# Optimization experiments

Measured on AMD Instinct MI355X. Metric: run time of the kernel, lower is better.

Reference implementation:

```python
import jax, jax.numpy as jnp
import numpy as np

N, G, E, R = 32768, 2048, 1146880, 3
NIN, GIN, F, OUT = 6, 4, 64, 1


def _w(k, fan_in, fan_out):
    return (jax.random.normal(k, (fan_in, fan_out), jnp.float32) / np.sqrt(fan_in)).astype(jnp.float32)


def setup_inputs() -> dict:
    key = jax.random.key(0)
    ks = jax.random.split(key, 20)
    x = jax.random.normal(ks[0], (N, NIN), jnp.float32)
    u = jax.random.normal(ks[1], (G, GIN), jnp.float32)
    batch = jnp.sort(jax.random.randint(ks[2], (N,), 0, G))
    hyperedge_index = jax.random.randint(ks[3], (R, E), 0, N)
    batch_hyper = jnp.sort(jax.random.randint(ks[4], (E,), 0, G))
    inp = {
        "x": x, "u": u, "batch": batch,
        "hyperedge_index": hyperedge_index, "batch_hyper": batch_hyper, "r": R,
        # mlp_x: (NIN+GIN)->F->F->F
        "W1": _w(ks[5], NIN + GIN, F), "b1": jnp.zeros((F,), jnp.float32),
        "W2": _w(ks[6], F, F), "b2": jnp.zeros((F,), jnp.float32),
        "W3": _w(ks[7], F, F), "b3": jnp.zeros((F,), jnp.float32),
        # weighting matrix [F,F]
        "weight": _w(ks[8], F, F),
        # x_hat: 2F->F->F->OUT
        "V1": _w(ks[9], 2 * F, F), "c1": jnp.zeros((F,), jnp.float32),
        "V2": _w(ks[10], F, F), "c2": jnp.zeros((F,), jnp.float32),
        "V3": _w(ks[11], F, OUT), "c3": jnp.zeros((OUT,), jnp.float32),
    }
    return inp


def _segment_softmax(x, idx, num_segments):
    # torch_geometric-style softmax grouped by idx along dim 0, per feature
    seg_max = jax.ops.segment_max(x, idx, num_segments=num_segments)
    ex = jnp.exp(x - seg_max[idx])
    denom = jax.ops.segment_sum(ex, idx, num_segments=num_segments)
    return ex / denom[idx]


def reference(x, u, batch, hyperedge_index, batch_hyper, r,
              W1, b1, W2, b2, W3, b3, weight, V1, c1, V2, c2, V3, c3):
    # mlp_x on [node_feats || global_feats_of_node's_graph]
    h = jnp.concatenate([x, u[batch]], axis=1)            # [N, NIN+GIN]
    h = jnp.maximum(h @ W1 + b1, 0.0)
    h = jnp.maximum(h @ W2 + b2, 0.0)
    h = h @ W3 + b3                                        # [N, F]

    # hyperedge finding: sum the r member-node embeddings of each hyperedge
    x_hyper = jnp.zeros((hyperedge_index.shape[1], h.shape[1]), h.dtype)
    for i in range(hyperedge_index.shape[0]):              # r is small & fixed
        x_hyper = x_hyper + jnp.take(h, hyperedge_index[i], axis=0)  # [E, F]

    # weighting: segment softmax over hyperedges of the same graph
    coef = _segment_softmax(x_hyper, batch_hyper, G)       # [E, F]
    x_hyper_hat = coef * jnp.maximum(x_hyper @ weight, 0.0)

    # x_hat head
    o = jnp.concatenate([x_hyper, x_hyper_hat], axis=1)    # [E, 2F]
    o = jnp.maximum(o @ V1 + c1, 0.0)
    o = jnp.maximum(o @ V2 + c2, 0.0)
    o = jax.nn.sigmoid(o @ V3 + c3)                        # [E, OUT]
    return (o, batch_hyper)
```

## Files before the change

### kernel.cpp

```cpp
#include <hip/hip_runtime.h>
#include <math.h>

typedef short bf16x8 __attribute__((ext_vector_type(8)));
typedef float f32x4  __attribute__((ext_vector_type(4)));
typedef unsigned short u16;
typedef unsigned int   u32;

#define MFMA16 __builtin_amdgcn_mfma_f32_16x16x32_bf16

__device__ __forceinline__ u16 f2b(float x) {
    union { float f; unsigned u; } v; v.f = x;
    unsigned r = v.u + 0x7fffu + ((v.u >> 16) & 1u);
    return (u16)(r >> 16);
}
__device__ __forceinline__ float b2f(u16 h) {
    union { unsigned u; float f; } v; v.u = ((unsigned)h) << 16;
    return v.f;
}
__device__ __forceinline__ float blo(u32 w) {
    union { u32 u; float f; } v; v.u = w << 16; return v.f;
}
__device__ __forceinline__ float bhi(u32 w) {
    union { u32 u; float f; } v; v.u = w & 0xffff0000u; return v.f;
}
__device__ __forceinline__ u32 add3pack(u32 x, u32 y, u32 z) {
    float lo = blo(x) + blo(y) + blo(z);
    float hi = bhi(x) + bhi(y) + bhi(z);
    return (u32)f2b(lo) | ((u32)f2b(hi) << 16);
}

__global__ __launch_bounds__(256) void prep_kernel(
    const float* __restrict__ Wg, const float* __restrict__ V1g,
    const float* __restrict__ V2g, u16* __restrict__ SWZ,
    const int* __restrict__ bh, int E, int G, int* __restrict__ seg_start)
{
    const int b = blockIdx.x, tid = threadIdx.x;
    if (b < 32) {
        int idx = b * 256 + tid;
        int k = idx >> 6, n = idx & 63;
        int off = ((k >> 5) * 4 + (n >> 4)) * 640 + (n & 15) * 40 + ((k >> 3) & 3) * 8 + (k & 7);
        SWZ[5120 + off] = f2b(V1g[idx]);
        if (idx < 4096) {
            SWZ[off]         = f2b(Wg[idx]);
            SWZ[15360 + off] = f2b(V2g[idx]);
        }
    } else {
        int g = (b - 32) * 256 + tid;
        if (g > G) return;
        int lo = 0, hi = E;
        while (lo < hi) {
            int mid = (lo + hi) >> 1;
            if (bh[mid] < g) lo = mid + 1; else hi = mid;
        }
        seg_start[g] = lo;
    }
}

__global__ __launch_bounds__(256) void node_mlp_kernel(
    const float* __restrict__ x, const float* __restrict__ u,
    const int* __restrict__ batch,
    const float* __restrict__ W1, const float* __restrict__ b1,
    const float* __restrict__ W2, const float* __restrict__ b2,
    const float* __restrict__ W3, const float* __restrict__ b3,
    u16* __restrict__ hb, int N)
{
    __shared__ float inbuf[4][10];
    __shared__ float h1[4][64];
    __shared__ float h2[4][64];
    const int tid = threadIdx.x;
    const int ni = tid >> 6, f = tid & 63;
    int node = blockIdx.x * 4 + ni;
    if (node >= N) node = N - 1;
    if (f < 6)       inbuf[ni][f] = x[node * 6 + f];
    else if (f < 10) inbuf[ni][f] = u[batch[node] * 4 + (f - 6)];
    __syncthreads();
    float acc = b1[f];
    #pragma unroll
    for (int k = 0; k < 10; ++k) acc = fmaf(inbuf[ni][k], W1[k * 64 + f], acc);
    h1[ni][f] = fmaxf(acc, 0.f);
    __syncthreads();
    acc = b2[f];
    #pragma unroll
    for (int k4 = 0; k4 < 16; ++k4) {
        float4 hv = *(const float4*)&h1[ni][k4 * 4];
        acc = fmaf(hv.x, W2[(k4 * 4 + 0) * 64 + f], acc);
        acc = fmaf(hv.y, W2[(k4 * 4 + 1) * 64 + f], acc);
        acc = fmaf(hv.z, W2[(k4 * 4 + 2) * 64 + f], acc);
        acc = fmaf(hv.w, W2[(k4 * 4 + 3) * 64 + f], acc);
    }
    h2[ni][f] = fmaxf(acc, 0.f);
    __syncthreads();
    acc = b3[f];
    #pragma unroll
    for (int k4 = 0; k4 < 16; ++k4) {
        float4 hv = *(const float4*)&h2[ni][k4 * 4];
        acc = fmaf(hv.x, W3[(k4 * 4 + 0) * 64 + f], acc);
        acc = fmaf(hv.y, W3[(k4 * 4 + 1) * 64 + f], acc);
        acc = fmaf(hv.z, W3[(k4 * 4 + 2) * 64 + f], acc);
        acc = fmaf(hv.w, W3[(k4 * 4 + 3) * 64 + f], acc);
    }
    hb[node * 64 + f] = f2b(acc);
}

__global__ __launch_bounds__(256) void gather_stats_kernel(
    const u16* __restrict__ hb, const int* __restrict__ hidx,
    const int* __restrict__ seg_start,
    u16* __restrict__ Xh, float* __restrict__ Sinv,
    float* __restrict__ out, int E)
{
    __shared__ float ps[4][16][4];
    const int tid = threadIdx.x, lane = tid & 63, wid = tid >> 6;
    const int sub = lane >> 4, cl = lane & 15;
    const int g = blockIdx.x;
    const int e0 = seg_start[g], e1 = seg_start[g + 1];
    if (e1 <= e0) return;
    const int e1m1 = e1 - 1;
    const float gf = (float)g;

    for (int e = e0 + tid; e < e1; e += 256) out[E + e] = gf;

    float s0 = 0.f, s1 = 0.f, s2 = 0.f, s3 = 0.f;
    for (int e = e0 + wid * 4 + sub; e < e1; e += 128) {
        #pragma unroll
        for (int j = 0; j < 8; ++j) {
            int ee = e + j * 16;
            int ec = min(ee, e1m1);
            int i0 = hidx[ec], i1 = hidx[E + ec], i2 = hidx[2 * E + ec];
            uint2 A0 = *(const uint2*)(hb + (size_t)i0 * 64 + cl * 4);
            uint2 A1 = *(const uint2*)(hb + (size_t)i1 * 64 + cl * 4);
            uint2 A2 = *(const uint2*)(hb + (size_t)i2 * 64 + cl * 4);
            u32 wx = add3pack(A0.x, A1.x, A2.x);
            u32 wy = add3pack(A0.y, A1.y, A2.y);
            if (ee < e1) {
                uint2 W; W.x = wx; W.y = wy;
                *(uint2*)(Xh + (size_t)ee * 64 + cl * 4) = W;
                s0 += __expf(blo(wx)); s1 += __expf(bhi(wx));
                s2 += __expf(blo(wy)); s3 += __expf(bhi(wy));
            }
        }
    }
    s0 += __shfl_xor(s0, 16); s0 += __shfl_xor(s0, 32);
    s1 += __shfl_xor(s1, 16); s1 += __shfl_xor(s1, 32);
    s2 += __shfl_xor(s2, 16); s2 += __shfl_xor(s2, 32);
    s3 += __shfl_xor(s3, 16); s3 += __shfl_xor(s3, 32);
    if (lane < 16) {
        ps[wid][cl][0] = s0; ps[wid][cl][1] = s1;
        ps[wid][cl][2] = s2; ps[wid][cl][3] = s3;
    }
    __syncthreads();
    if (tid < 64) {
        int c4 = tid >> 2, cc = tid & 3;
        float S = ps[0][c4][cc] + ps[1][c4][cc] + ps[2][c4][cc] + ps[3][c4][cc];
        Sinv[g * 64 + tid] = 1.f / S;
    }
}

__global__ __launch_bounds__(256, 3) void mfma_seg_kernel(
    const u16* __restrict__ Xh, const int* __restrict__ seg_start,
    const u16* __restrict__ SWZ, const float* __restrict__ Sinv,
    const float* __restrict__ c1g, const float* __restrict__ c2g,
    const float* __restrict__ V3g, const float* __restrict__ c3g,
    float* __restrict__ out, int E)
{
    __shared__ u16 SW[20480];
    __shared__ u16 XT_all[4][16 * 72];

    const int tid = threadIdx.x, lane = tid & 63, wid = tid >> 6;
    const int nl = lane & 15, rq = lane >> 4;
    const int g = blockIdx.x;
    const int e0 = seg_start[g], e1 = seg_start[g + 1];
    const int L = e1 - e0;
    if (L <= 0) return;
    const int e1m1 = e1 - 1;

    {
        const uint4* src = (const uint4*)SWZ;
        uint4* dst = (uint4*)SW;
        for (int i = tid; i < 2560; i += 256) dst[i] = src[i];
    }
    __syncthreads();
    const u16* WB  = SW;
    const u16* V1B = SW + 5120;
    const u16* V2B = SW + 15360;

    bf16x8 I0, I1;
    #pragma unroll
    for (int j = 0; j < 8; ++j) {
        I0[j] = (rq * 8 + j == nl)      ? (short)0x3F80 : (short)0;
        I1[j] = (rq * 8 + j == nl + 16) ? (short)0x3F80 : (short)0;
    }

    float dinvv[4], c1v[4], c2v[4], v3v[4];
    #pragma unroll
    for (int nt = 0; nt < 4; ++nt) {
        int col = nt * 16 + nl;
        dinvv[nt] = Sinv[g * 64 + col];
        c1v[nt]   = c1g[col];
        c2v[nt]   = c2g[col];
        v3v[nt]   = V3g[col];
    }
    const float c3s = c3g[0];
    u16* XT = XT_all[wid];
    const f32x4 zf = {0.f, 0.f, 0.f, 0.f};

    auto loadA = [&](int tt, bf16x8& A0, bf16x8& A1) {
        const u16* xp = Xh + (size_t)min(e0 + tt * 16 + nl, e1m1) * 64 + rq * 8;
        A0 = *(const bf16x8*)(xp);
        A1 = *(const bf16x8*)(xp + 32);
    };

    int t = wid;
    bf16x8 p0 = {}, p1 = {};
    if (t * 16 < L) loadA(t, p0, p1);

    for (; t * 16 < L; t += 8) {
        const int eB1 = e0 + t * 16;
        const int eB2 = eB1 + 64;

        bf16x8 a0 = p0, a1 = p1;
        bf16x8 a2, a3;
        loadA(t + 4, a2, a3);
        if ((t + 8) * 16 < L) loadA(t + 8, p0, p1);

        f32x4 xc1[4], xc2[4];
        xc1[0] = MFMA16(a0, I0, zf, 0, 0, 0);
        xc1[1] = MFMA16(a0, I1, zf, 0, 0, 0);
        xc1[2] = MFMA16(a1, I0, zf, 0, 0, 0);
        xc1[3] = MFMA16(a1, I1, zf, 0, 0, 0);
        xc2[0] = MFMA16(a2, I0, zf, 0, 0, 0);
        xc2[1] = MFMA16(a2, I1, zf, 0, 0, 0);
        xc2[2] = MFMA16(a3, I0, zf, 0, 0, 0);
        xc2[3] = MFMA16(a3, I1, zf, 0, 0, 0);

        f32x4 acc1[4] = {zf, zf, zf, zf}, acc2t[4] = {zf, zf, zf, zf};
        #pragma unroll
        for (int nt = 0; nt < 4; ++nt) {
            bf16x8 b0 = *(const bf16x8*)(WB + (0 * 4 + nt) * 640 + nl * 40 + rq * 8);
            acc1[nt]  = MFMA16(a0, b0, acc1[nt], 0, 0, 0);
            acc2t[nt] = MFMA16(a2, b0, acc2t[nt], 0, 0, 0);
            bf16x8 b1 = *(const bf16x8*)(WB + (1 * 4 + nt) * 640 + nl * 40 + rq * 8);
            acc1[nt]  = MFMA16(a1, b1, acc1[nt], 0, 0, 0);
            acc2t[nt] = MFMA16(a3, b1, acc2t[nt], 0, 0, 0);
        }
        #pragma unroll
        for (int nt = 0; nt < 4; ++nt) {
            #pragma unroll
            for (int r = 0; r < 4; ++r) {
                float coef = __expf(xc1[nt][r]) * dinvv[nt];
                XT[(rq * 4 + r) * 72 + nt * 16 + nl] =
                    f2b(coef * fmaxf(acc1[nt][r], 0.f));
            }
        }
        bf16x8 x2a = *(const bf16x8*)(XT + nl * 72 + rq * 8);
        bf16x8 x3a = *(const bf16x8*)(XT + nl * 72 + 32 + rq * 8);
        #pragma unroll
        for (int nt = 0; nt < 4; ++nt) {
            #pragma unroll
            for (int r = 0; r < 4; ++r) {
                float coef = __expf(xc2[nt][r]) * dinvv[nt];
                XT[(rq * 4 + r) * 72 + nt * 16 + nl] =
                    f2b(coef * fmaxf(acc2t[nt][r], 0.f));
            }
        }
        bf16x8 x2b = *(const bf16x8*)(XT + nl * 72 + rq * 8);
        bf16x8 x3b = *(const bf16x8*)(XT + nl * 72 + 32 + rq * 8);

        f32x4 va[4], vb[4];
        #pragma unroll
        for (int nt = 0; nt < 4; ++nt) {
            va[nt][0] = c1v[nt]; va[nt][1] = c1v[nt];
            va[nt][2] = c1v[nt]; va[nt][3] = c1v[nt];
            vb[nt] = va[nt];
        }
        #pragma unroll
        for (int nt = 0; nt < 4; ++nt) {
            bf16x8 b0 = *(const bf16x8*)(V1B + (0 * 4 + nt) * 640 + nl * 40 + rq * 8);
            va[nt] = MFMA16(a0, b0, va[nt], 0, 0, 0);
            vb[nt] = MFMA16(a2, b0, vb[nt], 0, 0, 0);
            bf16x8 b1 = *(const bf16x8*)(V1B + (1 * 4 + nt) * 640 + nl * 40 + rq * 8);
            va[nt] = MFMA16(a1, b1, va[nt], 0, 0, 0);
            vb[nt] = MFMA16(a3, b1, vb[nt], 0, 0, 0);
        }
        #pragma unroll
        for (int nt = 0; nt < 4; ++nt) {
            bf16x8 b2 = *(const bf16x8*)(V1B + (2 * 4 + nt) * 640 + nl * 40 + rq * 8);
            va[nt] = MFMA16(x2a, b2, va[nt], 0, 0, 0);
            vb[nt] = MFMA16(x2b, b2, vb[nt], 0, 0, 0);
            bf16x8 b3 = *(const bf16x8*)(V1B + (3 * 4 + nt) * 640 + nl * 40 + rq * 8);
            va[nt] = MFMA16(x3a, b3, va[nt], 0, 0, 0);
            vb[nt] = MFMA16(x3b, b3, vb[nt], 0, 0, 0);
        }
        #pragma unroll
        for (int nt = 0; nt < 4; ++nt) {
            #pragma unroll
            for (int r = 0; r < 4; ++r)
                XT[(rq * 4 + r) * 72 + nt * 16 + nl] = f2b(fmaxf(va[nt][r], 0.f));
        }
        bf16x8 o0a = *(const bf16x8*)(XT + nl * 72 + rq * 8);
        bf16x8 o1a = *(const bf16x8*)(XT + nl * 72 + 32 + rq * 8);
        #pragma unroll
        for (int nt = 0; nt < 4; ++nt) {
            #pragma unroll
            for (int r = 0; r < 4; ++r)
                XT[(rq * 4 + r) * 72 + nt * 16 + nl] = f2b(fmaxf(vb[nt][r], 0.f));
        }
        bf16x8 o0b = *(const bf16x8*)(XT + nl * 72 + rq * 8);
        bf16x8 o1b = *(const bf16x8*)(XT + nl * 72 + 32 + rq * 8);

        f32x4 wa[4], wb2[4];
        #pragma unroll
        for (int nt = 0; nt < 4; ++nt) {
            wa[nt][0] = c2v[nt]; wa[nt][1] = c2v[nt];
            wa[nt][2] = c2v[nt]; wa[nt][3] = c2v[nt];
            wb2[nt] = wa[nt];
        }
        #pragma unroll
        for (int nt = 0; nt < 4; ++nt) {
            bf16x8 b0 = *(const bf16x8*)(V2B + (0 * 4 + nt) * 640 + nl * 40 + rq * 8);
            wa[nt]  = MFMA16(o0a, b0, wa[nt], 0, 0, 0);
            wb2[nt] = MFMA16(o0b, b0, wb2[nt], 0, 0, 0);
            bf16x8 b1 = *(const bf16x8*)(V2B + (1 * 4 + nt) * 640 + nl * 40 + rq * 8);
            wa[nt]  = MFMA16(o1a, b1, wa[nt], 0, 0, 0);
            wb2[nt] = MFMA16(o1b, b1, wb2[nt], 0, 0, 0);
        }

        float sra[4], srb[4];
        #pragma unroll
        for (int r = 0; r < 4; ++r) {
            float u1 = 0.f, u2 = 0.f;
            #pragma unroll
            for (int nt = 0; nt < 4; ++nt) {
                u1 = fmaf(fmaxf(wa[nt][r],  0.f), v3v[nt], u1);
                u2 = fmaf(fmaxf(wb2[nt][r], 0.f), v3v[nt], u2);
            }
            u1 += __shfl_xor(u1, 1); u2 += __shfl_xor(u2, 1);
            u1 += __shfl_xor(u1, 2); u2 += __shfl_xor(u2, 2);
            u1 += __shfl_xor(u1, 4); u2 += __shfl_xor(u2, 4);
            u1 += __shfl_xor(u1, 8); u2 += __shfl_xor(u2, 8);
            sra[r] = u1; srb[r] = u2;
        }
        if (nl == 0) {
            #pragma unroll
            for (int r = 0; r < 4; ++r) {
                int ea = eB1 + rq * 4 + r;
                if (ea < e1) out[ea] = 1.f / (1.f + __expf(-(sra[r] + c3s)));
                int eb = eB2 + rq * 4 + r;
                if (eb < e1) out[eb] = 1.f / (1.f + __expf(-(srb[r] + c3s)));
            }
        }
    }
}

extern "C" void kernel_launch(void* const* d_in, const int* in_sizes, int n_in,
                              void* d_out, int out_size, void* d_ws, size_t ws_size,
                              hipStream_t stream) {
    const float* x     = (const float*)d_in[0];
    const float* u     = (const float*)d_in[1];
    const int*   batch = (const int*)  d_in[2];
    const int*   hidx  = (const int*)  d_in[3];
    const int*   bh    = (const int*)  d_in[4];
    const float* W1 = (const float*)d_in[6];
    const float* b1 = (const float*)d_in[7];
    const float* W2 = (const float*)d_in[8];
    const float* b2 = (const float*)d_in[9];
    const float* W3 = (const float*)d_in[10];
    const float* b3 = (const float*)d_in[11];
    const float* Wg = (const float*)d_in[12];
    const float* V1 = (const float*)d_in[13];
    const float* c1 = (const float*)d_in[14];
    const float* V2 = (const float*)d_in[15];
    const float* c2 = (const float*)d_in[16];
    const float* V3 = (const float*)d_in[17];
    const float* c3 = (const float*)d_in[18];

    const int N = in_sizes[0] / 6;
    const int G = in_sizes[1] / 4;
    const int E = in_sizes[4];

    char* ws = (char*)d_ws;
    size_t off = 0;
    u16* hb = (u16*)(ws + off);            off += (size_t)N * 64 * 2;
    int* seg_start = (int*)(ws + off);     off += ((size_t)G + 1) * 4;
    off = (off + 255) & ~(size_t)255;
    u16* SWZ = (u16*)(ws + off);           off += 20480 * 2;
    float* Sinv = (float*)(ws + off);      off += (size_t)G * 64 * 4;
    off = (off + 255) & ~(size_t)255;
    u16* Xh = (u16*)(ws + off);            off += (size_t)E * 64 * 2;
    float* out = (float*)d_out;

    const int prep_blocks = 32 + (G + 256) / 256;
    prep_kernel<<<prep_blocks, 256, 0, stream>>>(Wg, V1, V2, SWZ, bh, E, G, seg_start);
    node_mlp_kernel<<<(N + 3) / 4, 256, 0, stream>>>(
        x, u, batch, W1, b1, W2, b2, W3, b3, hb, N);
    gather_stats_kernel<<<G, 256, 0, stream>>>(hb, hidx, seg_start, Xh, Sinv, out, E);
    mfma_seg_kernel<<<G, 256, 0, stream>>>(
        Xh, seg_start, SWZ, Sinv, c1, c2, V3, c3, out, E);
}
```

Before: 280.1 us.

## Batch node MLP over 16 nodes, widen gather loads, pad LDS tile

```diff
diff --git a/kernel.cpp b/kernel.cpp
--- a/kernel.cpp
+++ b/kernel.cpp
@@ -12,6 +12,10 @@
     union { float f; unsigned u; } v; v.f = x;
     unsigned r = v.u + 0x7fffu + ((v.u >> 16) & 1u);
     return (u16)(r >> 16);
+}
+__device__ __forceinline__ u16 f2bu(float x) {
+    union { float f; unsigned u; } v; v.f = x;
+    return (u16)((v.u + 0x8000u) >> 16);
 }
 __device__ __forceinline__ float b2f(u16 h) {
     union { unsigned u; float f; } v; v.u = ((unsigned)h) << 16;
@@ -64,42 +68,71 @@
     const float* __restrict__ W3, const float* __restrict__ b3,
     u16* __restrict__ hb, int N)
 {
-    __shared__ float inbuf[4][10];
-    __shared__ float h1[4][64];
-    __shared__ float h2[4][64];
+    __shared__ float inbuf[16][10];
+    __shared__ float h1[16][64];
+    __shared__ float h2[16][64];
     const int tid = threadIdx.x;
     const int ni = tid >> 6, f = tid & 63;
-    int node = blockIdx.x * 4 + ni;
-    if (node >= N) node = N - 1;
-    if (f < 6)       inbuf[ni][f] = x[node * 6 + f];
-    else if (f < 10) inbuf[ni][f] = u[batch[node] * 4 + (f - 6)];
+    const int base = blockIdx.x * 16;
+    int nodes[4];
+    #pragma unroll
+    for (int s = 0; s < 4; ++s) {
+        nodes[s] = min(base + s * 4 + ni, N - 1);
+        if (f < 6)       inbuf[s * 4 + ni][f] = x[nodes[s] * 6 + f];
+        else if (f < 10) inbuf[s * 4 + ni][f] = u[batch[nodes[s]] * 4 + (f - 6)];
+    }
     __syncthreads();
-    float acc = b1[f];
-    #pragma unroll
-    for (int k = 0; k < 10; ++k) acc = fmaf(inbuf[ni][k], W1[k * 64 + f], acc);
-    h1[ni][f] = fmaxf(acc, 0.f);
+    float acc[4];
+    #pragma unroll
+    for (int s = 0; s < 4; ++s) acc[s] = b1[f];
+    #pragma unroll
+    for (int k = 0; k < 10; ++k) {
+        float w = W1[k * 64 + f];
+        #pragma unroll
+        for (int s = 0; s < 4; ++s) acc[s] = fmaf(inbuf[s * 4 + ni][k], w, acc[s]);
+    }
+    #pragma unroll
+    for (int s = 0; s < 4; ++s) h1[s * 4 + ni][f] = fmaxf(acc[s], 0.f);
     __syncthreads();
-    acc = b2[f];
+    #pragma unroll
+    for (int s = 0; s < 4; ++s) acc[s] = b2[f];
     #pragma unroll
     for (int k4 = 0; k4 < 16; ++k4) {
-        float4 hv = *(const float4*)&h1[ni][k4 * 4];
-        acc = fmaf(hv.x, W2[(k4 * 4 + 0) * 64 + f], acc);
-        acc = fmaf(hv.y, W2[(k4 * 4 + 1) * 64 + f], acc);
-        acc = fmaf(hv.z, W2[(k4 * 4 + 2) * 64 + f], acc);
-        acc = fmaf(hv.w, W2[(k4 * 4 + 3) * 64 + f], acc);
-    }
-    h2[ni][f] = fmaxf(acc, 0.f);
+        float w0 = W2[(k4 * 4 + 0) * 64 + f];
+        float w1 = W2[(k4 * 4 + 1) * 64 + f];
+        float w2 = W2[(k4 * 4 + 2) * 64 + f];
+        float w3 = W2[(k4 * 4 + 3) * 64 + f];
+        #pragma unroll
+        for (int s = 0; s < 4; ++s) {
+            float4 hv = *(const float4*)&h1[s * 4 + ni][k4 * 4];
+            acc[s] = fmaf(hv.x, w0, acc[s]);
+            acc[s] = fmaf(hv.y, w1, acc[s]);
+            acc[s] = fmaf(hv.z, w2, acc[s]);
+            acc[s] = fmaf(hv.w, w3, acc[s]);
+        }
+    }
+    #pragma unroll
+    for (int s = 0; s < 4; ++s) h2[s * 4 + ni][f] = fmaxf(acc[s], 0.f);
     __syncthreads();
-    acc = b3[f];
+    #pragma unroll
+    for (int s = 0; s < 4; ++s) acc[s] = b3[f];
     #pragma unroll
     for (int k4 = 0; k4 < 16; ++k4) {
-        float4 hv = *(const float4*)&h2[ni][k4 * 4];
-        acc = fmaf(hv.x, W3[(k4 * 4 + 0) * 64 + f], acc);
-        acc = fmaf(hv.y, W3[(k4 * 4 + 1) * 64 + f], acc);
-        acc = fmaf(hv.z, W3[(k4 * 4 + 2) * 64 + f], acc);
-        acc = fmaf(hv.w, W3[(k4 * 4 + 3) * 64 + f], acc);
-    }
-    hb[node * 64 + f] = f2b(acc);
+        float w0 = W3[(k4 * 4 + 0) * 64 + f];
+        float w1 = W3[(k4 * 4 + 1) * 64 + f];
+        float w2 = W3[(k4 * 4 + 2) * 64 + f];
+        float w3 = W3[(k4 * 4 + 3) * 64 + f];
+        #pragma unroll
+        for (int s = 0; s < 4; ++s) {
+            float4 hv = *(const float4*)&h2[s * 4 + ni][k4 * 4];
+            acc[s] = fmaf(hv.x, w0, acc[s]);
+            acc[s] = fmaf(hv.y, w1, acc[s]);
+            acc[s] = fmaf(hv.z, w2, acc[s]);
+            acc[s] = fmaf(hv.w, w3, acc[s]);
+        }
+    }
+    #pragma unroll
+    for (int s = 0; s < 4; ++s) hb[nodes[s] * 64 + f] = f2b(acc[s]);
 }
 
 __global__ __launch_bounds__(256) void gather_stats_kernel(
@@ -108,9 +141,9 @@
     u16* __restrict__ Xh, float* __restrict__ Sinv,
     float* __restrict__ out, int E)
 {
-    __shared__ float ps[4][16][4];
+    __shared__ float ps[4][8][8];
     const int tid = threadIdx.x, lane = tid & 63, wid = tid >> 6;
-    const int sub = lane >> 4, cl = lane & 15;
+    const int sub = lane >> 3, cl = lane & 7;
     const int g = blockIdx.x;
     const int e0 = seg_start[g], e1 = seg_start[g + 1];
     if (e1 <= e0) return;
@@ -119,38 +152,44 @@
 
     for (int e = e0 + tid; e < e1; e += 256) out[E + e] = gf;
 
-    float s0 = 0.f, s1 = 0.f, s2 = 0.f, s3 = 0.f;
-    for (int e = e0 + wid * 4 + sub; e < e1; e += 128) {
-        #pragma unroll
-        for (int j = 0; j < 8; ++j) {
-            int ee = e + j * 16;
+    float s[8] = {0.f, 0.f, 0.f, 0.f, 0.f, 0.f, 0.f, 0.f};
+    for (int e = e0 + wid * 8 + sub; e < e1; e += 128) {
+        #pragma unroll
+        for (int j = 0; j < 4; ++j) {
+            int ee = e + j * 32;
             int ec = min(ee, e1m1);
             int i0 = hidx[ec], i1 = hidx[E + ec], i2 = hidx[2 * E + ec];
-            uint2 A0 = *(const uint2*)(hb + (size_t)i0 * 64 + cl * 4);
-            uint2 A1 = *(const uint2*)(hb + (size_t)i1 * 64 + cl * 4);
-            uint2 A2 = *(const uint2*)(hb + (size_t)i2 * 64 + cl * 4);
-            u32 wx = add3pack(A0.x, A1.x, A2.x);
-            u32 wy = add3pack(A0.y, A1.y, A2.y);
+            uint4 A0 = *(const uint4*)(hb + (size_t)i0 * 64 + cl * 8);
+            uint4 A1 = *(const uint4*)(hb + (size_t)i1 * 64 + cl * 8);
+            uint4 A2 = *(const uint4*)(hb + (size_t)i2 * 64 + cl * 8);
+            u32 w0 = add3pack(A0.x, A1.x, A2.x);
+            u32 w1 = add3pack(A0.y, A1.y, A2.y);
+            u32 w2 = add3pack(A0.z, A1.z, A2.z);
+            u32 w3 = add3pack(A0.w, A1.w, A2.w);
             if (ee < e1) {
-                uint2 W; W.x = wx; W.y = wy;
-                *(uint2*)(Xh + (size_t)ee * 64 + cl * 4) = W;
-                s0 += __expf(blo(wx)); s1 += __expf(bhi(wx));
-                s2 += __expf(blo(wy)); s3 += __expf(bhi(wy));
+                uint4 W; W.x = w0; W.y = w1; W.z = w2; W.w = w3;
+                *(uint4*)(Xh + (size_t)ee * 64 + cl * 8) = W;
+                s[0] += __expf(blo(w0)); s[1] += __expf(bhi(w0));
+                s[2] += __expf(blo(w1)); s[3] += __expf(bhi(w1));
+                s[4] += __expf(blo(w2)); s[5] += __expf(bhi(w2));
+                s[6] += __expf(blo(w3)); s[7] += __expf(bhi(w3));
             }
         }
     }
-    s0 += __shfl_xor(s0, 16); s0 += __shfl_xor(s0, 32);
-    s1 += __shfl_xor(s1, 16); s1 += __shfl_xor(s1, 32);
-    s2 += __shfl_xor(s2, 16); s2 += __shfl_xor(s2, 32);
-    s3 += __shfl_xor(s3, 16); s3 += __shfl_xor(s3, 32);
-    if (lane < 16) {
-        ps[wid][cl][0] = s0; ps[wid][cl][1] = s1;
-        ps[wid][cl][2] = s2; ps[wid][cl][3] = s3;
+    #pragma unroll
+    for (int k = 0; k < 8; ++k) {
+        s[k] += __shfl_xor(s[k], 8);
+        s[k] += __shfl_xor(s[k], 16);
+        s[k] += __shfl_xor(s[k], 32);
+    }
+    if (lane < 8) {
+        #pragma unroll
+        for (int k = 0; k < 8; ++k) ps[wid][lane][k] = s[k];
     }
     __syncthreads();
     if (tid < 64) {
-        int c4 = tid >> 2, cc = tid & 3;
-        float S = ps[0][c4][cc] + ps[1][c4][cc] + ps[2][c4][cc] + ps[3][c4][cc];
+        int c8 = tid >> 3, cc = tid & 7;
+        float S = ps[0][c8][cc] + ps[1][c8][cc] + ps[2][c8][cc] + ps[3][c8][cc];
         Sinv[g * 64 + tid] = 1.f / S;
     }
 }
@@ -163,7 +202,7 @@
     float* __restrict__ out, int E)
 {
     __shared__ u16 SW[20480];
-    __shared__ u16 XT_all[4][16 * 72];
+    __shared__ u16 XT_all[4][16 * 76];
 
     const int tid = threadIdx.x, lane = tid & 63, wid = tid >> 6;
     const int nl = lane & 15, rq = lane >> 4;
@@ -247,23 +286,23 @@
             #pragma unroll
             for (int r = 0; r < 4; ++r) {
                 float coef = __expf(xc1[nt][r]) * dinvv[nt];
-                XT[(rq * 4 + r) * 72 + nt * 16 + nl] =
-                    f2b(coef * fmaxf(acc1[nt][r], 0.f));
+                XT[(rq * 4 + r) * 76 + nt * 16 + nl] =
+                    f2bu(coef * fmaxf(acc1[nt][r], 0.f));
             }
         }
-        bf16x8 x2a = *(const bf16x8*)(XT + nl * 72 + rq * 8);
-        bf16x8 x3a = *(const bf16x8*)(XT + nl * 72 + 32 + rq * 8);
+        bf16x8 x2a = *(const bf16x8*)(XT + nl * 76 + rq * 8);
+        bf16x8 x3a = *(const bf16x8*)(XT + nl * 76 + 32 + rq * 8);
         #pragma unroll
         for (int nt = 0; nt < 4; ++nt) {
             #pragma unroll
             for (int r = 0; r < 4; ++r) {
                 float coef = __expf(xc2[nt][r]) * dinvv[nt];
-                XT[(rq * 4 + r) * 72 + nt * 16 + nl] =
-                    f2b(coef * fmaxf(acc2t[nt][r], 0.f));
+                XT[(rq * 4 + r) * 76 + nt * 16 + nl] =
+                    f2bu(coef * fmaxf(acc2t[nt][r], 0.f));
             }
         }
-        bf16x8 x2b = *(const bf16x8*)(XT + nl * 72 + rq * 8);
-        bf16x8 x3b = *(const bf16x8*)(XT + nl * 72 + 32 + rq * 8);
+        bf16x8 x2b = *(const bf16x8*)(XT + nl * 76 + rq * 8);
+        bf16x8 x3b = *(const bf16x8*)(XT + nl * 76 + 32 + rq * 8);
 
         f32x4 va[4], vb[4];
         #pragma unroll
@@ -294,18 +333,18 @@
         for (int nt = 0; nt < 4; ++nt) {
             #pragma unroll
             for (int r = 0; r < 4; ++r)
-                XT[(rq * 4 + r) * 72 + nt * 16 + nl] = f2b(fmaxf(va[nt][r], 0.f));
-        }
-        bf16x8 o0a = *(const bf16x8*)(XT + nl * 72 + rq * 8);
-        bf16x8 o1a = *(const bf16x8*)(XT + nl * 72 + 32 + rq * 8);
+                XT[(rq * 4 + r) * 76 + nt * 16 + nl] = f2bu(fmaxf(va[nt][r], 0.f));
+        }
+        bf16x8 o0a = *(const bf16x8*)(XT + nl * 76 + rq * 8);
+        bf16x8 o1a = *(const bf16x8*)(XT + nl * 76 + 32 + rq * 8);
         #pragma unroll
         for (int nt = 0; nt < 4; ++nt) {
             #pragma unroll
             for (int r = 0; r < 4; ++r)
-                XT[(rq * 4 + r) * 72 + nt * 16 + nl] = f2b(fmaxf(vb[nt][r], 0.f));
-        }
-        bf16x8 o0b = *(const bf16x8*)(XT + nl * 72 + rq * 8);
-        bf16x8 o1b = *(const bf16x8*)(XT + nl * 72 + 32 + rq * 8);
+                XT[(rq * 4 + r) * 76 + nt * 16 + nl] = f2bu(fmaxf(vb[nt][r], 0.f));
+        }
+        bf16x8 o0b = *(const bf16x8*)(XT + nl * 76 + rq * 8);
+        bf16x8 o1b = *(const bf16x8*)(XT + nl * 76 + 32 + rq * 8);
 
         f32x4 wa[4], wb2[4];
         #pragma unroll
@@ -390,7 +429,7 @@
 
     const int prep_blocks = 32 + (G + 256) / 256;
     prep_kernel<<<prep_blocks, 256, 0, stream>>>(Wg, V1, V2, SWZ, bh, E, G, seg_start);
-    node_mlp_kernel<<<(N + 3) / 4, 256, 0, stream>>>(
+    node_mlp_kernel<<<(N + 15) / 16, 256, 0, stream>>>(
         x, u, batch, W1, b1, W2, b2, W3, b3, hb, N);
     gather_stats_kernel<<<G, 256, 0, stream>>>(hb, hidx, seg_start, Xh, Sinv, out, E);
     mfma_seg_kernel<<<G, 256, 0, stream>>>(
```

Result: faster. 270.3 us (-3.5%).
